# Performance work log

Hardware: AMD Instinct MI355X
Metric: run time of the kernel (lower is better)

The kernel has to match this reference:

```python
import jax, jax.numpy as jnp
import numpy as np

B, N, DIM, H, DH = 8, 1024, 512, 8, 64
INNER = H * DH
SCALE = DH ** -0.5


def setup_inputs() -> dict:
    key = jax.random.key(0)
    ks = jax.random.split(key, 9)
    s = 0.02
    return {
        "x": jax.random.normal(ks[0], (B, N, DIM), jnp.float32),
        "lidar": jax.random.normal(ks[1], (B, N, INNER), jnp.float32),
        "w_qkv": jax.random.normal(ks[2], (3 * INNER, DIM), jnp.float32) * s,
        "w_merge": jax.random.normal(ks[3], (DH, DH), jnp.float32) * s,
        "b_merge": jnp.zeros((DH,), jnp.float32),
        "w_out": jax.random.normal(ks[4], (DIM, INNER), jnp.float32) * s,
        "b_out": jnp.zeros((DIM,), jnp.float32),
        "conv_w": jax.random.normal(ks[5], (2,), jnp.float32) * 0.5,
        "conv_b": jnp.zeros((), jnp.float32),
    }


def _split_heads(t):  # [b, n, h*d] -> [b, h, n, d]
    b, n, _ = t.shape
    return t.reshape(b, n, H, DH).transpose(0, 2, 1, 3)


def reference(x, lidar, w_qkv, w_merge, b_merge, w_out, b_out, conv_w, conv_b):
    b, n, _ = x.shape
    qkv = x @ w_qkv.T  # [b, n, 3*inner]
    q, k, v = jnp.split(qkv, 3, axis=-1)
    q, k, v = _split_heads(q), _split_heads(k), _split_heads(v)
    lid = _split_heads(lidar)

    dots = jnp.einsum('bhid,bhjd->bhij', q, k) * SCALE
    lidar_sim = jnp.einsum('bhid,bhjd->bhij', lid, lid) * SCALE
    lidar_sim = jax.nn.softmax(lidar_sim, axis=-1)

    # 1x1 conv over 2 channels == learned linear blend of the two score maps
    mid = conv_w[0] * dots + conv_w[1] * lidar_sim + conv_b
    attn = jax.nn.softmax(mid, axis=-1)

    out = jnp.einsum('bhij,bhjd->bhid', attn, v)
    out = out @ w_merge.T + b_merge                  # per-head linear_merge
    out = out.transpose(0, 2, 1, 3).reshape(b, n, INNER)  # b h n d -> b n (h d)
    out = out @ w_out.T + b_out                      # to_out (dropout = identity)
    return (out, lidar)
```

## Files before the change

### kernel.cpp

```cpp
#include <hip/hip_runtime.h>
#include <hip/hip_bf16.h>

#define B_      8
#define N_      1024
#define DIM_    512
#define H_      8
#define DH_     64
#define INNER_  512
#define SCALE_  0.125f
#define LOG2E_  1.4426950408889634f

typedef __attribute__((ext_vector_type(8))) __bf16         bf16x8;
typedef __attribute__((ext_vector_type(8))) unsigned short ushort8;
typedef __attribute__((ext_vector_type(4))) float          f32x4;

union FragCast { ushort8 u; bf16x8 b; };
union FragU32  { unsigned int u[4]; bf16x8 b; };

__device__ inline bf16x8 ld_frag(const unsigned short* p) {
    FragCast f; f.u = *(const ushort8*)p; return f.b;
}

__device__ inline f32x4 mfma16(bf16x8 a, bf16x8 b, f32x4 c) {
    return __builtin_amdgcn_mfma_f32_16x16x32_bf16(a, b, c, 0, 0, 0);
}

__device__ inline float fexp2(float x) { return __builtin_amdgcn_exp2f(x); }

__device__ inline unsigned short f2bf(float x) {
    unsigned int u = __float_as_uint(x);
    unsigned int lsb = (u >> 16) & 1u;
    u += 0x7fffu + lsb;
    return (unsigned short)(u >> 16);
}

__device__ inline unsigned int pack_bf2(float hi, float lo) {
    return __builtin_amdgcn_perm(__float_as_uint(hi), __float_as_uint(lo), 0x07060302u);
}

__device__ inline void gl_lds(const unsigned short* g, unsigned short* l) {
    __builtin_amdgcn_global_load_lds(
        (const __attribute__((address_space(1))) unsigned int*)g,
        (__attribute__((address_space(3))) unsigned int*)l, 16, 0, 0);
}

__global__ __launch_bounds__(256) void k_convert(
    const float* __restrict__ x, const float* __restrict__ lidar,
    const float* __restrict__ wqkv, const float* __restrict__ wmerge,
    const float* __restrict__ wout,
    unsigned short* __restrict__ x_bf, unsigned short* __restrict__ lid_bf,
    float* __restrict__ out_lidar,
    unsigned short* __restrict__ wqkv_bf, unsigned short* __restrict__ wm_bf,
    unsigned short* __restrict__ wout_bf)
{
    const int bx = blockIdx.x, tid = threadIdx.x;
    const float* src; unsigned short* dst; bool isLid = false; long base;
    if (bx < 1024)      { src = x;      dst = x_bf;    base = (long)bx * 1024; }
    else if (bx < 2048) { src = lidar;  dst = lid_bf;  base = (long)(bx - 1024) * 1024; isLid = true; }
    else if (bx < 2240) { src = wqkv;   dst = wqkv_bf; base = (long)(bx - 2048) * 1024; }
    else if (bx < 2304) { src = wout;   dst = wout_bf; base = (long)(bx - 2240) * 1024; }
    else                { src = wmerge; dst = wm_bf;   base = 0; }
    for (int k = 0; k < 4; k++) {
        long j = base + k * 256 + tid;
        float4 v = ((const float4*)src)[j];
        ushort4 o;
        o.x = f2bf(v.x); o.y = f2bf(v.y); o.z = f2bf(v.z); o.w = f2bf(v.w);
        ((ushort4*)dst)[j] = o;
        if (isLid) ((float4*)out_lidar)[j] = v;
    }
}

__global__ __launch_bounds__(256) void k_gemm_qkv(
    const unsigned short* __restrict__ A, const unsigned short* __restrict__ Bm,
    unsigned short* __restrict__ C, unsigned short* __restrict__ vt,
    int M, int Nd, int K)
{
    __shared__ unsigned short sMem[128 * 136];
    unsigned short* sA = sMem;
    unsigned short* sB = sMem + 128 * 64;
    const int tid  = threadIdx.x;
    const int lane = tid & 63, wave = tid >> 6;
    const int q = lane >> 4, l15 = lane & 15, l7 = l15 & 7;
    const int xq0 = (q ^ l7) << 3, xq4 = ((q + 4) ^ l7) << 3;
    const int m0 = blockIdx.x * 128, n0 = blockIdx.y * 128;
    const int wm = (wave >> 1) * 64, wn = (wave & 1) * 64;
    f32x4 acc[4][4] = {};

    for (int k0 = 0; k0 < K; k0 += 64) {
        __syncthreads();
        for (int i = 0; i < 4; i++) {
            int c = i * 256 + tid;
            int row = c >> 3;
            int gcol = ((c & 7) ^ (row & 7)) << 3;
            gl_lds(&A[(long)(m0 + row) * K + k0 + gcol], &sA[c * 8]);
            gl_lds(&Bm[(long)(n0 + row) * K + k0 + gcol], &sB[c * 8]);
        }
        __syncthreads();
        for (int kk = 0; kk < 2; kk++) {
            const int xx = kk ? xq4 : xq0;
            bf16x8 af[4], bfr[4];
            for (int i = 0; i < 4; i++)
                af[i]  = ld_frag(&sA[(wm + i * 16 + l15) * 64 + xx]);
            for (int i = 0; i < 4; i++)
                bfr[i] = ld_frag(&sB[(wn + i * 16 + l15) * 64 + xx]);
            for (int mi = 0; mi < 4; mi++)
                for (int ni = 0; ni < 4; ni++)
                    acc[mi][ni] = mfma16(af[mi], bfr[ni], acc[mi][ni]);
        }
    }
    if (n0 < 1024) {
        for (int mi = 0; mi < 4; mi++)
            for (int ni = 0; ni < 4; ni++)
                for (int r = 0; r < 4; r++) {
                    int row = m0 + wm + mi * 16 + q * 4 + r;
                    int col = n0 + wn + ni * 16 + l15;
                    C[(long)row * Nd + col] = f2bf(acc[mi][ni][r]);
                }
    } else {
        __syncthreads();
        for (int mi = 0; mi < 4; mi++) {
            int t0 = wm + mi * 16 + q * 4;
            for (int ni = 0; ni < 4; ni++) {
                int f = wn + ni * 16 + l15;
                ushort4 o4;
                o4.x = f2bf(acc[mi][ni][0]); o4.y = f2bf(acc[mi][ni][1]);
                o4.z = f2bf(acc[mi][ni][2]); o4.w = f2bf(acc[mi][ni][3]);
                *(ushort4*)&sMem[f * 136 + t0] = o4;
            }
        }
        __syncthreads();
        const long fb = (long)(n0 - 1024) * (B_ * N_) + m0;
        for (int i = 0; i < 8; i++) {
            int g = i * 256 + tid;
            int f = g >> 4, grp = g & 15;
            int base = (grp >> 2) * 32 + (grp & 3) * 4;
            ushort4 a4 = *(const ushort4*)&sMem[f * 136 + base];
            ushort4 b4 = *(const ushort4*)&sMem[f * 136 + base + 16];
            ushort8 o8 = {a4.x, a4.y, a4.z, a4.w, b4.x, b4.y, b4.z, b4.w};
            *(ushort8*)&vt[fb + (long)f * (B_ * N_) + grp * 8] = o8;
        }
    }
}

__global__ __launch_bounds__(256) void k_gemm_out(
    const unsigned short* __restrict__ A, const unsigned short* __restrict__ Bm,
    const float* __restrict__ bias, float* __restrict__ C, int M, int Nd, int K)
{
    __shared__ unsigned short sA[128 * 64];
    __shared__ unsigned short sB[64 * 64];
    const int tid  = threadIdx.x;
    const int lane = tid & 63, wave = tid >> 6;
    const int q = lane >> 4, l15 = lane & 15, l7 = l15 & 7;
    const int xq0 = (q ^ l7) << 3, xq4 = ((q + 4) ^ l7) << 3;
    const int m0 = blockIdx.x * 128, n0 = blockIdx.y * 64;
    const int wm = (wave >> 1) * 64, wn = (wave & 1) * 32;
    f32x4 acc[4][2] = {};

    for (int k0 = 0; k0 < K; k0 += 64) {
        __syncthreads();
        for (int i = 0; i < 4; i++) {
            int c = i * 256 + tid;
            int row = c >> 3;
            int gcol = ((c & 7) ^ (row & 7)) << 3;
            gl_lds(&A[(long)(m0 + row) * K + k0 + gcol], &sA[c * 8]);
            if (i < 2)
                gl_lds(&Bm[(long)(n0 + row) * K + k0 + gcol], &sB[c * 8]);
        }
        __syncthreads();
        for (int kk = 0; kk < 2; kk++) {
            const int xx = kk ? xq4 : xq0;
            bf16x8 af[4], bfr[2];
            for (int i = 0; i < 4; i++)
                af[i]  = ld_frag(&sA[(wm + i * 16 + l15) * 64 + xx]);
            for (int i = 0; i < 2; i++)
                bfr[i] = ld_frag(&sB[(wn + i * 16 + l15) * 64 + xx]);
            for (int mi = 0; mi < 4; mi++)
                for (int ni = 0; ni < 2; ni++)
                    acc[mi][ni] = mfma16(af[mi], bfr[ni], acc[mi][ni]);
        }
    }
    for (int mi = 0; mi < 4; mi++)
        for (int ni = 0; ni < 2; ni++)
            for (int r = 0; r < 4; r++) {
                int row = m0 + wm + mi * 16 + q * 4 + r;
                int col = n0 + wn + ni * 16 + l15;
                C[(long)row * Nd + col] = acc[mi][ni][r] + bias[col];
            }
}

__global__ __launch_bounds__(256) void k_flash(
    const unsigned short* __restrict__ qkv_bf, const unsigned short* __restrict__ lid_bf,
    const unsigned short* __restrict__ vt,
    const unsigned short* __restrict__ wm_bf, const float* __restrict__ b_merge,
    const float* __restrict__ conv_w, const float* __restrict__ conv_b,
    unsigned short* __restrict__ tmp_bf)
{
    __shared__ unsigned short sK[64 * 64];
    __shared__ unsigned short sLid[64 * 64];
    __shared__ unsigned short sVT[64 * 64];
    __shared__ unsigned short sO[4 * 16 * 72];
    __shared__ float sRS[4][16];

    const int tid = threadIdx.x, lane = tid & 63, wave = tid >> 6;
    const int q = lane >> 4, l15 = lane & 15, l7 = l15 & 7;
    const int xq0 = (q ^ l7) << 3, xq4 = ((q + 4) ^ l7) << 3;
    const int bh = blockIdx.x, itile = blockIdx.y;
    const int b = bh >> 3, h = bh & 7;
    const int i0w = itile * 64 + wave * 16;
    const long rowB = (long)b * N_;
    const int colh = h * DH_;
    const float k0c = conv_w[0] * SCALE_ * LOG2E_;
    const float k2c = conv_b[0] * LOG2E_;
    const float c1L = conv_w[1] * LOG2E_;
    const float sc = SCALE_ * LOG2E_;

    int c0i = tid, c1i = 256 + tid;
    int row0 = c0i >> 3, row1 = c1i >> 3;
    int gc0 = ((c0i & 7) ^ (row0 & 7)) << 3;
    int gc1 = ((c1i & 7) ^ (row1 & 7)) << 3;
    unsigned short* dK0 = &sK[c0i * 8];   unsigned short* dK1 = &sK[c1i * 8];
    unsigned short* dL0 = &sLid[c0i * 8]; unsigned short* dL1 = &sLid[c1i * 8];
    unsigned short* dV0 = &sVT[c0i * 8];  unsigned short* dV1 = &sVT[c1i * 8];
    const unsigned short* gK0 = &qkv_bf[(rowB + row0) * 1536 + 512 + colh + gc0];
    const unsigned short* gK1 = &qkv_bf[(rowB + row1) * 1536 + 512 + colh + gc1];
    const unsigned short* gL0 = &lid_bf[(rowB + row0) * INNER_ + colh + gc0];
    const unsigned short* gL1 = &lid_bf[(rowB + row1) * INNER_ + colh + gc1];
    const unsigned short* gV0 = &vt[(long)(colh + row0) * (B_ * N_) + rowB + gc0];
    const unsigned short* gV1 = &vt[(long)(colh + row1) * (B_ * N_) + rowB + gc1];

    const unsigned short *sK_r[4], *sL_r[4];
    for (int ns = 0; ns < 4; ns++) {
        sK_r[ns] = &sK[(ns * 16 + l15) * 64];
        sL_r[ns] = &sLid[(ns * 16 + l15) * 64];
    }

    bf16x8 qf[2], lfq[2];
    for (int ks = 0; ks < 2; ks++) {
        qf[ks]  = ld_frag(&qkv_bf[(rowB + i0w + l15) * 1536 + colh + ks * 32 + q * 8]);
        lfq[ks] = ld_frag(&lid_bf[(rowB + i0w + l15) * INNER_ + colh + ks * 32 + q * 8]);
    }

    float rsl = 0.f;
    {
        const unsigned short* p0 = gL0;
        const unsigned short* p1 = gL1;
        for (int j0 = 0; j0 < N_; j0 += 64) {
            __syncthreads();
            gl_lds(p0, dL0);
            gl_lds(p1, dL1);
            p0 += 64 * INNER_; p1 += 64 * INNER_;
            __syncthreads();
            for (int ns = 0; ns < 4; ns++) {
                f32x4 cv = {0.f, 0.f, 0.f, 0.f};
                cv = mfma16(ld_frag(sL_r[ns] + xq0), lfq[0], cv);
                cv = mfma16(ld_frag(sL_r[ns] + xq4), lfq[1], cv);
                for (int r = 0; r < 4; r++) rsl += fexp2(cv[r] * sc);
            }
        }
    }
    rsl += __shfl_xor(rsl, 16);
    rsl += __shfl_xor(rsl, 32);
    const float k1 = c1L / rsl;

    float rs = 0.f;
    f32x4 o[4] = {};

    for (int j0 = 0; j0 < N_; j0 += 64) {
        __syncthreads();
        gl_lds(gK0, dK0); gl_lds(gK1, dK1);
        gl_lds(gL0, dL0); gl_lds(gL1, dL1);
        gl_lds(gV0, dV0); gl_lds(gV1, dV1);
        gK0 += 64 * 1536;  gK1 += 64 * 1536;
        gL0 += 64 * INNER_; gL1 += 64 * INNER_;
        gV0 += 64;          gV1 += 64;
        __syncthreads();

        for (int ns2 = 0; ns2 < 2; ns2++) {
            FragU32 fa;
            for (int h2 = 0; h2 < 2; h2++) {
                int ns = ns2 * 2 + h2;
                f32x4 a = {0.f, 0.f, 0.f, 0.f};
                a = mfma16(ld_frag(sK_r[ns] + xq0), qf[0], a);
                a = mfma16(ld_frag(sK_r[ns] + xq4), qf[1], a);
                f32x4 cv = {0.f, 0.f, 0.f, 0.f};
                cv = mfma16(ld_frag(sL_r[ns] + xq0), lfq[0], cv);
                cv = mfma16(ld_frag(sL_r[ns] + xq4), lfq[1], cv);
                float pv[4];
                for (int r = 0; r < 4; r++) {
                    float els = fexp2(cv[r] * sc);
                    float t = fmaf(k0c, a[r], k2c);
                    t = fmaf(k1, els, t);
                    pv[r] = fexp2(t);
                    rs += pv[r];
                }
                fa.u[h2 * 2 + 0] = pack_bf2(pv[1], pv[0]);
                fa.u[h2 * 2 + 1] = pack_bf2(pv[3], pv[2]);
            }
            for (int dt = 0; dt < 4; dt++) {
                int vrow = dt * 16 + l15;
                bf16x8 vb = ld_frag(&sVT[vrow * 64 + (((ns2 * 4 + q) ^ l7) << 3)]);
                o[dt] = mfma16(fa.b, vb, o[dt]);
            }
        }
    }

    rs += __shfl_xor(rs, 16);
    rs += __shfl_xor(rs, 32);
    if (q == 0) sRS[wave][l15] = rs;
    float invr[4];
    for (int r = 0; r < 4; r++) invr[r] = 1.f / sRS[wave][q * 4 + r];

    unsigned short* pO = &sO[wave * 16 * 72];
    for (int dt = 0; dt < 4; dt++)
        for (int r = 0; r < 4; r++)
            pO[(q * 4 + r) * 72 + dt * 16 + l15] = f2bf(o[dt][r] * invr[r]);

    f32x4 mo[4] = {};
    for (int ks = 0; ks < 2; ks++) {
        bf16x8 af = ld_frag(&pO[l15 * 72 + ks * 32 + q * 8]);
        for (int ns = 0; ns < 4; ns++) {
            bf16x8 wf = ld_frag(&wm_bf[(ns * 16 + l15) * 64 + ks * 32 + q * 8]);
            mo[ns] = mfma16(af, wf, mo[ns]);
        }
    }
    for (int ns = 0; ns < 4; ns++) {
        float bm = b_merge[ns * 16 + l15];
        for (int r = 0; r < 4; r++) {
            long row = rowB + i0w + q * 4 + r;
            tmp_bf[row * INNER_ + colh + ns * 16 + l15] = f2bf(mo[ns][r] + bm);
        }
    }
}

extern "C" void kernel_launch(void* const* d_in, const int* in_sizes, int n_in,
                              void* d_out, int out_size, void* d_ws, size_t ws_size,
                              hipStream_t stream) {
    const float* x       = (const float*)d_in[0];
    const float* lidar   = (const float*)d_in[1];
    const float* w_qkv   = (const float*)d_in[2];
    const float* w_merge = (const float*)d_in[3];
    const float* b_merge = (const float*)d_in[4];
    const float* w_out   = (const float*)d_in[5];
    const float* b_out   = (const float*)d_in[6];
    const float* conv_w  = (const float*)d_in[7];
    const float* conv_b  = (const float*)d_in[8];

    float* out0      = (float*)d_out;
    float* out_lidar = out0 + (long)B_ * N_ * INNER_;

    size_t off = 0;
    auto carve = [&](size_t bytes) {
        void* p = (char*)d_ws + off;
        off += (bytes + 255) & ~(size_t)255;
        return p;
    };
    unsigned short* qkv_bf  = (unsigned short*)carve((size_t)B_ * N_ * 3 * INNER_ * 2);
    unsigned short* lid_bf  = (unsigned short*)carve((size_t)B_ * N_ * INNER_ * 2);
    unsigned short* x_bf    = (unsigned short*)carve((size_t)B_ * N_ * DIM_ * 2);
    unsigned short* wqkv_bf = (unsigned short*)carve((size_t)3 * INNER_ * DIM_ * 2);
    unsigned short* wout_bf = (unsigned short*)carve((size_t)DIM_ * INNER_ * 2);
    unsigned short* wm_bf   = (unsigned short*)carve((size_t)DH_ * DH_ * 2);
    unsigned short* tmp_bf  = (unsigned short*)carve((size_t)B_ * N_ * INNER_ * 2);
    unsigned short* vt_bf   = (unsigned short*)carve((size_t)INNER_ * B_ * N_ * 2);

    k_convert<<<2305, 256, 0, stream>>>(x, lidar, w_qkv, w_merge, w_out,
                                        x_bf, lid_bf, out_lidar,
                                        wqkv_bf, wm_bf, wout_bf);

    k_gemm_qkv<<<dim3(64, 12), 256, 0, stream>>>(
        x_bf, wqkv_bf, qkv_bf, vt_bf, B_ * N_, 3 * INNER_, DIM_);

    k_flash<<<dim3(64, 16), 256, 0, stream>>>(
        qkv_bf, lid_bf, vt_bf, wm_bf, b_merge, conv_w, conv_b, tmp_bf);

    k_gemm_out<<<dim3(64, 8), 256, 0, stream>>>(
        tmp_bf, wout_bf, b_out, out0, B_ * N_, DIM_, INNER_);
}
```

Baseline: 193.8 us.

## Fuse fp32-to-bf16 conversion into QKV GEMM and merge with remaining conversions

The QKV projection now reads fp32 x and w_qkv directly, converting them to bf16 in registers before writing to padded LDS. This removes the separate x/w_qkv conversion pass and its bf16 round trip through memory. The remaining conversions (lidar, w_out, w_merge) run as extra blocks of the same launch, so one kernel launch disappears. In exchange, the async global_load_lds path and the swizzled layout give way to register-staged loads with a padded stride. The GEMM also re-reads fp32 operands, which doubles the load bytes per tile.

```diff
diff --git a/kernel.cpp b/kernel.cpp
--- a/kernel.cpp
+++ b/kernel.cpp
@@ -44,77 +44,79 @@
         (__attribute__((address_space(3))) unsigned int*)l, 16, 0, 0);
 }
 
-__global__ __launch_bounds__(256) void k_convert(
-    const float* __restrict__ x, const float* __restrict__ lidar,
-    const float* __restrict__ wqkv, const float* __restrict__ wmerge,
+__global__ __launch_bounds__(256) void k_front(
+    const float* __restrict__ x, const float* __restrict__ wqkv,
+    const float* __restrict__ lidar, const float* __restrict__ wmerge,
     const float* __restrict__ wout,
-    unsigned short* __restrict__ x_bf, unsigned short* __restrict__ lid_bf,
-    float* __restrict__ out_lidar,
-    unsigned short* __restrict__ wqkv_bf, unsigned short* __restrict__ wm_bf,
-    unsigned short* __restrict__ wout_bf)
+    unsigned short* __restrict__ qkv_bf, unsigned short* __restrict__ vt,
+    unsigned short* __restrict__ lid_bf, float* __restrict__ out_lidar,
+    unsigned short* __restrict__ wm_bf, unsigned short* __restrict__ wout_bf)
 {
-    const int bx = blockIdx.x, tid = threadIdx.x;
-    const float* src; unsigned short* dst; bool isLid = false; long base;
-    if (bx < 1024)      { src = x;      dst = x_bf;    base = (long)bx * 1024; }
-    else if (bx < 2048) { src = lidar;  dst = lid_bf;  base = (long)(bx - 1024) * 1024; isLid = true; }
-    else if (bx < 2240) { src = wqkv;   dst = wqkv_bf; base = (long)(bx - 2048) * 1024; }
-    else if (bx < 2304) { src = wout;   dst = wout_bf; base = (long)(bx - 2240) * 1024; }
-    else                { src = wmerge; dst = wm_bf;   base = 0; }
-    for (int k = 0; k < 4; k++) {
-        long j = base + k * 256 + tid;
-        float4 v = ((const float4*)src)[j];
-        ushort4 o;
-        o.x = f2bf(v.x); o.y = f2bf(v.y); o.z = f2bf(v.z); o.w = f2bf(v.w);
-        ((ushort4*)dst)[j] = o;
-        if (isLid) ((float4*)out_lidar)[j] = v;
-    }
-}
-
-__global__ __launch_bounds__(256) void k_gemm_qkv(
-    const unsigned short* __restrict__ A, const unsigned short* __restrict__ Bm,
-    unsigned short* __restrict__ C, unsigned short* __restrict__ vt,
-    int M, int Nd, int K)
-{
-    __shared__ unsigned short sMem[128 * 136];
+    __shared__ unsigned short sMem[128 * 144];
+    const int bid = blockIdx.x, tid = threadIdx.x;
+
+    if (bid >= 768) {
+        int cb = bid - 768;
+        const float* src; unsigned short* dst; bool isLid = false; long base;
+        if (cb < 1024)      { src = lidar;  dst = lid_bf;  base = (long)cb * 1024; isLid = true; }
+        else if (cb < 1088) { src = wout;   dst = wout_bf; base = (long)(cb - 1024) * 1024; }
+        else                { src = wmerge; dst = wm_bf;   base = 0; }
+        for (int k = 0; k < 4; k++) {
+            long j = base + k * 256 + tid;
+            float4 v = ((const float4*)src)[j];
+            ushort4 o;
+            o.x = f2bf(v.x); o.y = f2bf(v.y); o.z = f2bf(v.z); o.w = f2bf(v.w);
+            ((ushort4*)dst)[j] = o;
+            if (isLid) ((float4*)out_lidar)[j] = v;
+        }
+        return;
+    }
+
     unsigned short* sA = sMem;
-    unsigned short* sB = sMem + 128 * 64;
-    const int tid  = threadIdx.x;
+    unsigned short* sB = sMem + 128 * 72;
     const int lane = tid & 63, wave = tid >> 6;
-    const int q = lane >> 4, l15 = lane & 15, l7 = l15 & 7;
-    const int xq0 = (q ^ l7) << 3, xq4 = ((q + 4) ^ l7) << 3;
-    const int m0 = blockIdx.x * 128, n0 = blockIdx.y * 128;
+    const int q = lane >> 4, l15 = lane & 15;
+    const int mt = bid & 63, nt = bid >> 6;
+    const int m0 = mt * 128, n0 = nt * 128;
     const int wm = (wave >> 1) * 64, wn = (wave & 1) * 64;
+    const int rowg = tid >> 4, c4 = tid & 15;
     f32x4 acc[4][4] = {};
 
-    for (int k0 = 0; k0 < K; k0 += 64) {
-        __syncthreads();
-        for (int i = 0; i < 4; i++) {
-            int c = i * 256 + tid;
-            int row = c >> 3;
-            int gcol = ((c & 7) ^ (row & 7)) << 3;
-            gl_lds(&A[(long)(m0 + row) * K + k0 + gcol], &sA[c * 8]);
-            gl_lds(&Bm[(long)(n0 + row) * K + k0 + gcol], &sB[c * 8]);
-        }
-        __syncthreads();
-        for (int kk = 0; kk < 2; kk++) {
-            const int xx = kk ? xq4 : xq0;
+    for (int k0 = 0; k0 < 512; k0 += 64) {
+        float4 av[8], bv[8];
+        for (int p = 0; p < 8; p++) {
+            int row = p * 16 + rowg;
+            av[p] = *(const float4*)&x[(long)(m0 + row) * 512 + k0 + c4 * 4];
+            bv[p] = *(const float4*)&wqkv[(long)(n0 + row) * 512 + k0 + c4 * 4];
+        }
+        __syncthreads();
+        for (int p = 0; p < 8; p++) {
+            int row = p * 16 + rowg;
+            uint2 ua = { pack_bf2(av[p].y, av[p].x), pack_bf2(av[p].w, av[p].z) };
+            uint2 ub = { pack_bf2(bv[p].y, bv[p].x), pack_bf2(bv[p].w, bv[p].z) };
+            *(uint2*)&sA[row * 72 + c4 * 4] = ua;
+            *(uint2*)&sB[row * 72 + c4 * 4] = ub;
+        }
+        __syncthreads();
+        for (int kk = 0; kk < 64; kk += 32) {
             bf16x8 af[4], bfr[4];
             for (int i = 0; i < 4; i++)
-                af[i]  = ld_frag(&sA[(wm + i * 16 + l15) * 64 + xx]);
+                af[i]  = ld_frag(&sA[(wm + i * 16 + l15) * 72 + kk + q * 8]);
             for (int i = 0; i < 4; i++)
-                bfr[i] = ld_frag(&sB[(wn + i * 16 + l15) * 64 + xx]);
+                bfr[i] = ld_frag(&sB[(wn + i * 16 + l15) * 72 + kk + q * 8]);
             for (int mi = 0; mi < 4; mi++)
                 for (int ni = 0; ni < 4; ni++)
                     acc[mi][ni] = mfma16(af[mi], bfr[ni], acc[mi][ni]);
         }
     }
+
     if (n0 < 1024) {
         for (int mi = 0; mi < 4; mi++)
             for (int ni = 0; ni < 4; ni++)
                 for (int r = 0; r < 4; r++) {
                     int row = m0 + wm + mi * 16 + q * 4 + r;
                     int col = n0 + wn + ni * 16 + l15;
-                    C[(long)row * Nd + col] = f2bf(acc[mi][ni][r]);
+                    qkv_bf[(long)row * 1536 + col] = f2bf(acc[mi][ni][r]);
                 }
     } else {
         __syncthreads();
@@ -356,19 +358,14 @@
     };
     unsigned short* qkv_bf  = (unsigned short*)carve((size_t)B_ * N_ * 3 * INNER_ * 2);
     unsigned short* lid_bf  = (unsigned short*)carve((size_t)B_ * N_ * INNER_ * 2);
-    unsigned short* x_bf    = (unsigned short*)carve((size_t)B_ * N_ * DIM_ * 2);
-    unsigned short* wqkv_bf = (unsigned short*)carve((size_t)3 * INNER_ * DIM_ * 2);
     unsigned short* wout_bf = (unsigned short*)carve((size_t)DIM_ * INNER_ * 2);
     unsigned short* wm_bf   = (unsigned short*)carve((size_t)DH_ * DH_ * 2);
     unsigned short* tmp_bf  = (unsigned short*)carve((size_t)B_ * N_ * INNER_ * 2);
     unsigned short* vt_bf   = (unsigned short*)carve((size_t)INNER_ * B_ * N_ * 2);
 
-    k_convert<<<2305, 256, 0, stream>>>(x, lidar, w_qkv, w_merge, w_out,
-                                        x_bf, lid_bf, out_lidar,
-                                        wqkv_bf, wm_bf, wout_bf);
-
-    k_gemm_qkv<<<dim3(64, 12), 256, 0, stream>>>(
-        x_bf, wqkv_bf, qkv_bf, vt_bf, B_ * N_, 3 * INNER_, DIM_);
+    k_front<<<1857, 256, 0, stream>>>(
+        x, w_qkv, lidar, w_merge, w_out,
+        qkv_bf, vt_bf, lid_bf, out_lidar, wm_bf, wout_bf);
 
     k_flash<<<dim3(64, 16), 256, 0, stream>>>(
         qkv_bf, lid_bf, vt_bf, wm_bf, b_merge, conv_w, conv_b, tmp_bf);
```

Result: slower. 197.7 us (+2.0%).
